# Performance work log

Hardware: AMD Instinct MI355X
Metric: run time of the kernel (lower is better)

Reference implementation:

```python
import jax, jax.numpy as jnp
import numpy as np

EPS_COMBINE = 1e-6   # F.normalize eps in embedder
EPS_FINAL = 1e-12    # F.normalize default eps


def _l2norm(x, eps):
    # torch F.normalize: x / max(||x||_2, eps)
    n = jnp.sqrt(jnp.sum(x * x, axis=-1, keepdims=True))
    return x / jnp.maximum(n, eps)


def setup_inputs() -> dict:
    key = jax.random.key(0)
    ks = jax.random.split(key, 6)
    B, H, E = 16384, 768, 8
    s1 = 1.0 / np.sqrt(H)
    s2 = 1.0 / np.sqrt(H // 2)
    return {
        "embedding": jax.random.normal(ks[0], (B, H), jnp.float32),
        "gate_logits": jax.random.normal(ks[1], (B, E), jnp.float32),
        "W1": jax.random.normal(ks[2], (E, H, H // 2), jnp.float32) * s1,
        "b1": jax.random.normal(ks[3], (E, H // 2), jnp.float32) * s1,
        "W2": jax.random.normal(ks[4], (E, H // 2, H), jnp.float32) * s2,
        "b2": jax.random.normal(ks[5], (E, H), jnp.float32) * s2,
    }


def reference(embedding, gate_logits, W1, b1, W2, b2):
    # cls(): softmax + top-1 mask (sbmoe_top1)
    p = jax.nn.softmax(gate_logits, axis=-1)               # [B, E]
    mask = jax.nn.one_hot(jnp.argmax(p, axis=-1), p.shape[-1], dtype=p.dtype)
    gate = p * mask                                        # [B, E]

    # embedder(): run EVERY expert (2-layer MLP) on all samples
    h = jax.nn.relu(jnp.einsum('bd,edh->beh', embedding, W1) + b1[None])  # [B, E, H/2]
    embs = jnp.einsum('beh,ehd->bed', h, W2) + b2[None]                   # [B, E, H]

    # weighted combine + normalize + residual
    combined = jnp.einsum('bed,be->bd', embs, gate)        # [B, H]
    out = _l2norm(combined, EPS_COMBINE) + embedding
    # normalize=True
    return _l2norm(out, EPS_FINAL)
```

## Files before the change

### kernel.cpp

```cpp
#include <hip/hip_runtime.h>
#include <hip/hip_bf16.h>
#include <stdint.h>

#define B_N   16384
#define H_DIM 768
#define HH    384
#define NE    8
#define CSTRIDE 32

typedef __attribute__((ext_vector_type(8))) short bf16x8;
typedef __attribute__((ext_vector_type(4))) float f32x4;

__device__ __forceinline__ unsigned short f2bf(float f) {
    uint32_t u = __float_as_uint(f);
    return (unsigned short)((u + 0x7fffu + ((u >> 16) & 1u)) >> 16);
}

__global__ void zero_counts_kernel(int* __restrict__ counts) {
    if (threadIdx.x < NE) counts[threadIdx.x * CSTRIDE] = 0;
}

__global__ void route_kernel(const float* __restrict__ logits,
                             int* __restrict__ counts,
                             int* __restrict__ buckets) {
    __shared__ int lcnt[NE];
    __shared__ int lbase[NE];
    const int tid = threadIdx.x;
    if (tid < NE) lcnt[tid] = 0;
    __syncthreads();

    const int b = blockIdx.x * 256 + tid;
    const float* l = logits + (size_t)b * NE;
    float best = l[0];
    int be = 0;
#pragma unroll
    for (int e = 1; e < NE; ++e) {
        float v = l[e];
        if (v > best) { best = v; be = e; }
    }
    const int lpos = atomicAdd(&lcnt[be], 1);
    __syncthreads();
    if (tid < NE) lbase[tid] = atomicAdd(&counts[tid * CSTRIDE], lcnt[tid]);
    __syncthreads();
    buckets[be * B_N + lbase[be] + lpos] = b;
}

__global__ void transpose_cvt_kernel(const float* __restrict__ W1,
                                     const float* __restrict__ W2,
                                     unsigned short* __restrict__ W1T,
                                     unsigned short* __restrict__ W2T,
                                     int* __restrict__ counts) {
    if (blockIdx.x == 0 && blockIdx.y == 0 && blockIdx.z == 0 && threadIdx.x < NE)
        counts[threadIdx.x * CSTRIDE] = 0;

    const int z = blockIdx.z;
    const int R = z ? HH : H_DIM;
    const int C = z ? H_DIM : HH;
    const float* src = (z ? W2 : W1) + (size_t)blockIdx.y * R * C;
    unsigned short* dst = (z ? W2T : W1T) + (size_t)blockIdx.y * R * C;

    const int ctiles = C >> 5;
    const int ty = blockIdx.x / ctiles;
    const int tx = blockIdx.x % ctiles;

    __shared__ float Ts[32][33];
    const int lr = threadIdx.x >> 3;
    const int lc = (threadIdx.x & 7) * 4;

    f32x4 v = *reinterpret_cast<const f32x4*>(src + (size_t)(ty * 32 + lr) * C + tx * 32 + lc);
    Ts[lr][lc + 0] = v[0]; Ts[lr][lc + 1] = v[1];
    Ts[lr][lc + 2] = v[2]; Ts[lr][lc + 3] = v[3];
    __syncthreads();

    ushort4 o;
    o.x = f2bf(Ts[lc + 0][lr]);
    o.y = f2bf(Ts[lc + 1][lr]);
    o.z = f2bf(Ts[lc + 2][lr]);
    o.w = f2bf(Ts[lc + 3][lr]);
    *reinterpret_cast<ushort4*>(dst + (size_t)(tx * 32 + lr) * R + ty * 32 + lc) = o;
}

template<int KTOT, int NTOT, bool A_F32, bool RELU_BF16>
__global__ __launch_bounds__(256, 4)
void gemm_kernel(const void* __restrict__ Aglob,
                 const unsigned short* __restrict__ WT,
                 const float* __restrict__ bias,
                 const int* __restrict__ counts,
                 const int* __restrict__ buckets,
                 void* __restrict__ Cout) {
    __shared__ __align__(16) unsigned char AsB[64 * 128];
    __shared__ __align__(16) unsigned char BsB[128 * 128];
    __shared__ int sidx[64];

    const int e      = blockIdx.y;
    const int cnt    = counts[e * CSTRIDE];
    const int mtile  = blockIdx.x & 255;
    const int nchunk = blockIdx.x >> 8;
    const int base   = mtile * 64;
    if (base >= cnt) return;
    const int ns  = min(64, cnt - base);
    const int tid = threadIdx.x;

    if (tid < 64) sidx[tid] = buckets[e * B_N + base + (tid < ns ? tid : 0)];
    __syncthreads();

    const int ar = tid >> 2, aq = tid & 3;
    const int bn = tid >> 1, bh = tid & 1;
    const float*          arow_f = nullptr;
    const unsigned short* arow_h = nullptr;
    if (A_F32) arow_f = (const float*)Aglob + (size_t)sidx[ar] * KTOT;
    else       arow_h = (const unsigned short*)Aglob + (size_t)sidx[ar] * KTOT;
    const unsigned short* brow =
        WT + ((size_t)e * NTOT + nchunk * 128 + bn) * KTOT;

    const int w = tid >> 6, lane = tid & 63;
    const int wr = w >> 1, wc = w & 1;
    const int fr = lane & 15, fq = lane >> 4;

    f32x4 acc[2][4];
#pragma unroll
    for (int mi = 0; mi < 2; ++mi)
#pragma unroll
        for (int ni = 0; ni < 4; ++ni) acc[mi][ni] = (f32x4)(0.f);

    for (int k0 = 0; k0 < KTOT; k0 += 64) {
        if (A_F32) {
            const float* ap = arow_f + k0 + aq * 16;
            f32x4 f0 = *reinterpret_cast<const f32x4*>(ap + 0);
            f32x4 f1 = *reinterpret_cast<const f32x4*>(ap + 4);
            f32x4 f2 = *reinterpret_cast<const f32x4*>(ap + 8);
            f32x4 f3 = *reinterpret_cast<const f32x4*>(ap + 12);
            bf16x8 p0, p1;
#pragma unroll
            for (int i = 0; i < 4; ++i) {
                p0[i]     = (short)f2bf(f0[i]);
                p0[i + 4] = (short)f2bf(f1[i]);
                p1[i]     = (short)f2bf(f2[i]);
                p1[i + 4] = (short)f2bf(f3[i]);
            }
            const int kb0 = aq * 32, sw = (ar & 7) << 4;
            *reinterpret_cast<bf16x8*>(&AsB[(ar << 7) + ((kb0)      ^ sw)]) = p0;
            *reinterpret_cast<bf16x8*>(&AsB[(ar << 7) + ((kb0 + 16) ^ sw)]) = p1;
        } else {
            const unsigned short* ap = arow_h + k0 + aq * 16;
            f32x4 c0 = *reinterpret_cast<const f32x4*>(ap + 0);
            f32x4 c1 = *reinterpret_cast<const f32x4*>(ap + 8);
            const int kb0 = aq * 32, sw = (ar & 7) << 4;
            *reinterpret_cast<f32x4*>(&AsB[(ar << 7) + ((kb0)      ^ sw)]) = c0;
            *reinterpret_cast<f32x4*>(&AsB[(ar << 7) + ((kb0 + 16) ^ sw)]) = c1;
        }
        {
            const unsigned short* bp = brow + k0 + bh * 32;
            f32x4 c0 = *reinterpret_cast<const f32x4*>(bp + 0);
            f32x4 c1 = *reinterpret_cast<const f32x4*>(bp + 8);
            f32x4 c2 = *reinterpret_cast<const f32x4*>(bp + 16);
            f32x4 c3 = *reinterpret_cast<const f32x4*>(bp + 24);
            const int kb0 = bh * 64, sw = (bn & 7) << 4;
            *reinterpret_cast<f32x4*>(&BsB[(bn << 7) + ((kb0)      ^ sw)]) = c0;
            *reinterpret_cast<f32x4*>(&BsB[(bn << 7) + ((kb0 + 16) ^ sw)]) = c1;
            *reinterpret_cast<f32x4*>(&BsB[(bn << 7) + ((kb0 + 32) ^ sw)]) = c2;
            *reinterpret_cast<f32x4*>(&BsB[(bn << 7) + ((kb0 + 48) ^ sw)]) = c3;
        }
        __syncthreads();

#pragma unroll
        for (int s = 0; s < 2; ++s) {
            bf16x8 af[2], bf[4];
            const int kb = s * 64 + fq * 16;
#pragma unroll
            for (int mi = 0; mi < 2; ++mi) {
                int row = wr * 32 + mi * 16 + fr;
                af[mi] = *reinterpret_cast<const bf16x8*>(&AsB[(row << 7) + (kb ^ ((row & 7) << 4))]);
            }
#pragma unroll
            for (int ni = 0; ni < 4; ++ni) {
                int row = wc * 64 + ni * 16 + fr;
                bf[ni] = *reinterpret_cast<const bf16x8*>(&BsB[(row << 7) + (kb ^ ((row & 7) << 4))]);
            }
#pragma unroll
            for (int mi = 0; mi < 2; ++mi)
#pragma unroll
                for (int ni = 0; ni < 4; ++ni)
                    acc[mi][ni] = __builtin_amdgcn_mfma_f32_16x16x32_bf16(
                        af[mi], bf[ni], acc[mi][ni], 0, 0, 0);
        }
        __syncthreads();
    }

    const float* be = bias + (size_t)e * NTOT + nchunk * 128 + wc * 64;
#pragma unroll
    for (int mi = 0; mi < 2; ++mi) {
        const int rl0 = wr * 32 + mi * 16 + fq * 4;
        int  sid[4];
        bool val[4];
#pragma unroll
        for (int r2 = 0; r2 < 4; ++r2) {
            int rl = rl0 + r2;
            val[r2] = (rl < ns);
            sid[r2] = sidx[rl];
        }
#pragma unroll
        for (int ni = 0; ni < 4; ++ni) {
            const int coll = ni * 16 + fr;
            const int colg = nchunk * 128 + wc * 64 + coll;
            const float bb = be[coll];
#pragma unroll
            for (int r2 = 0; r2 < 4; ++r2) {
                float v = acc[mi][ni][r2] + bb;
                if (RELU_BF16) {
                    v = fmaxf(v, 0.f);
                    if (val[r2])
                        ((unsigned short*)Cout)[(size_t)sid[r2] * NTOT + colg] = f2bf(v);
                } else {
                    if (val[r2])
                        ((float*)Cout)[(size_t)sid[r2] * NTOT + colg] = v;
                }
            }
        }
    }
}

__global__ void norm_kernel(const float* __restrict__ emb, float* __restrict__ out) {
    const int row  = blockIdx.x * 4 + (threadIdx.x >> 6);
    const int lane = threadIdx.x & 63;
    float* y = out + (size_t)row * H_DIM;
    const float* x = emb + (size_t)row * H_DIM;

    f32x4 yv[3], xv[3];
    float s1 = 0.f, s2 = 0.f, s3 = 0.f;
#pragma unroll
    for (int c = 0; c < 3; ++c) {
        int col = c * 256 + lane * 4;
        yv[c] = *reinterpret_cast<const f32x4*>(y + col);
        xv[c] = *reinterpret_cast<const f32x4*>(x + col);
#pragma unroll
        for (int i = 0; i < 4; ++i) {
            s1 = fmaf(yv[c][i], yv[c][i], s1);
            s2 = fmaf(yv[c][i], xv[c][i], s2);
            s3 = fmaf(xv[c][i], xv[c][i], s3);
        }
    }
#pragma unroll
    for (int m = 1; m < 64; m <<= 1) {
        s1 += __shfl_xor(s1, m);
        s2 += __shfl_xor(s2, m);
        s3 += __shfl_xor(s3, m);
    }
    const float n1 = fmaxf(sqrtf(s1), 1e-6f);
    const float i1 = 1.f / n1;
    const float t  = s1 * i1 * i1 + 2.f * s2 * i1 + s3;
    const float i2 = 1.f / fmaxf(sqrtf(t), 1e-12f);
#pragma unroll
    for (int c = 0; c < 3; ++c) {
        int col = c * 256 + lane * 4;
        f32x4 o;
#pragma unroll
        for (int i = 0; i < 4; ++i) o[i] = (yv[c][i] * i1 + xv[c][i]) * i2;
        *reinterpret_cast<f32x4*>(y + col) = o;
    }
}

#define TILE 64
#define NTHR 256
#define BK   64
__global__ __launch_bounds__(NTHR, 2)
void moe_fused_fallback(const float* __restrict__ emb,
                        const float* __restrict__ W1,
                        const float* __restrict__ b1,
                        const float* __restrict__ W2,
                        const float* __restrict__ b2,
                        const int* __restrict__ counts,
                        const int* __restrict__ buckets,
                        float* __restrict__ out) {
    __shared__ float Xs[TILE][BK];
    __shared__ __hip_bfloat16 Hs[TILE][HH];
    __shared__ int   sidx[TILE];
    __shared__ float s_in1[TILE];
    __shared__ float s_in2[TILE];

    const int e    = blockIdx.y;
    const int cnt  = counts[e * CSTRIDE];
    const int base = blockIdx.x * TILE;
    if (base >= cnt) return;
    const int ns = min(TILE, cnt - base);
    const int tid = threadIdx.x;
    const int sg  = tid >> 5;
    const int cg  = tid & 31;

    if (tid < TILE) sidx[tid] = buckets[e * B_N + base + ((tid < ns) ? tid : 0)];
    __syncthreads();

    float acc[8][12];
#pragma unroll
    for (int i = 0; i < 8; ++i)
#pragma unroll
        for (int j = 0; j < 12; ++j) acc[i][j] = 0.f;

    const float* W1e = W1 + (size_t)e * H_DIM * HH;
    const int r = tid >> 2, q = tid & 3;
    const float* xrow = emb + (size_t)sidx[r] * H_DIM;

    for (int kk = 0; kk < H_DIM; kk += BK) {
#pragma unroll
        for (int i = 0; i < 4; ++i)
            *reinterpret_cast<float4*>(&Xs[r][q * 16 + i * 4]) =
                *reinterpret_cast<const float4*>(xrow + kk + q * 16 + i * 4);
        __syncthreads();
#pragma unroll 2
        for (int k = 0; k < BK; ++k) {
            float xv[8], wv[12];
            const float* wrow = W1e + (size_t)(kk + k) * HH + cg;
#pragma unroll
            for (int j = 0; j < 12; ++j) wv[j] = wrow[j * 32];
#pragma unroll
            for (int i = 0; i < 8; ++i) xv[i] = Xs[sg * 8 + i][k];
#pragma unroll
            for (int i = 0; i < 8; ++i)
#pragma unroll
                for (int j = 0; j < 12; ++j) acc[i][j] = fmaf(xv[i], wv[j], acc[i][j]);
        }
        __syncthreads();
    }
    const float* b1e = b1 + e * HH;
#pragma unroll
    for (int j = 0; j < 12; ++j) {
        float bb = b1e[cg + j * 32];
#pragma unroll
        for (int i = 0; i < 8; ++i)
            Hs[sg * 8 + i][cg + j * 32] = __float2bfloat16(fmaxf(acc[i][j] + bb, 0.f));
    }
    __syncthreads();

    const float* W2e = W2 + (size_t)e * HH * H_DIM;
    const float* b2e = b2 + e * H_DIM;
    float S1[8], S2[8], S3[8];
#pragma unroll
    for (int i = 0; i < 8; ++i) { S1[i] = 0.f; S2[i] = 0.f; S3[i] = 0.f; }

    for (int hb = 0; hb < H_DIM; hb += 384) {
        float acc2[8][12];
#pragma unroll
        for (int i = 0; i < 8; ++i)
#pragma unroll
            for (int j = 0; j < 12; ++j) acc2[i][j] = 0.f;
#pragma unroll 2
        for (int k = 0; k < HH; ++k) {
            float hv[8], wv[12];
            const float* wrow = W2e + (size_t)k * H_DIM + hb + cg;
#pragma unroll
            for (int j = 0; j < 12; ++j) wv[j] = wrow[j * 32];
#pragma unroll
            for (int i = 0; i < 8; ++i) hv[i] = __bfloat162float(Hs[sg * 8 + i][k]);
#pragma unroll
            for (int i = 0; i < 8; ++i)
#pragma unroll
                for (int j = 0; j < 12; ++j) acc2[i][j] = fmaf(hv[i], wv[j], acc2[i][j]);
        }
#pragma unroll
        for (int j = 0; j < 12; ++j) {
            int col = hb + cg + j * 32;
            float bb = b2e[col];
#pragma unroll
            for (int i = 0; i < 8; ++i) {
                int s = sg * 8 + i;
                float y = acc2[i][j] + bb;
                size_t o = (size_t)sidx[s] * H_DIM + col;
                float x = emb[o];
                S1[i] = fmaf(y, y, S1[i]);
                S2[i] = fmaf(y, x, S2[i]);
                S3[i] = fmaf(x, x, S3[i]);
                if (s < ns) out[o] = y;
            }
        }
    }
#pragma unroll
    for (int i = 0; i < 8; ++i) {
        float v1 = S1[i], v2 = S2[i], v3 = S3[i];
#pragma unroll
        for (int m = 1; m < 32; m <<= 1) {
            v1 += __shfl_xor(v1, m); v2 += __shfl_xor(v2, m); v3 += __shfl_xor(v3, m);
        }
        if (cg == 0) {
            float n1 = fmaxf(sqrtf(v1), 1e-6f);
            float t  = v1 / (n1 * n1) + 2.f * v2 / n1 + v3;
            s_in1[sg * 8 + i] = 1.f / n1;
            s_in2[sg * 8 + i] = 1.f / fmaxf(sqrtf(t), 1e-12f);
        }
    }
    __syncthreads();
#pragma unroll
    for (int i = 0; i < 8; ++i) {
        int s = sg * 8 + i;
        if (s >= ns) continue;
        float in1 = s_in1[s], in2 = s_in2[s];
        size_t rowo = (size_t)sidx[s] * H_DIM;
#pragma unroll
        for (int j = 0; j < 24; ++j) {
            int col = cg + j * 32;
            out[rowo + col] = (out[rowo + col] * in1 + emb[rowo + col]) * in2;
        }
    }
}

extern "C" void kernel_launch(void* const* d_in, const int* in_sizes, int n_in,
                              void* d_out, int out_size, void* d_ws, size_t ws_size,
                              hipStream_t stream) {
    const float* emb    = (const float*)d_in[0];
    const float* logits = (const float*)d_in[1];
    const float* W1     = (const float*)d_in[2];
    const float* b1     = (const float*)d_in[3];
    const float* W2     = (const float*)d_in[4];
    const float* b2     = (const float*)d_in[5];
    float* out = (float*)d_out;

    int* counts  = (int*)d_ws;
    int* buckets = (int*)((char*)d_ws + 1024);
    unsigned short* W1T = (unsigned short*)((char*)d_ws + 1024 + 524288);
    unsigned short* W2T = W1T + (size_t)NE * HH * H_DIM;
    unsigned short* Hws = W2T + (size_t)NE * HH * H_DIM;
    const size_t needed = 1024 + 524288
                        + 2 * (size_t)NE * HH * H_DIM * sizeof(unsigned short)
                        + (size_t)B_N * HH * sizeof(unsigned short);

    if (ws_size >= needed) {
        transpose_cvt_kernel<<<dim3(288, NE, 2), 256, 0, stream>>>(W1, W2, W1T, W2T, counts);
        route_kernel<<<B_N / 256, 256, 0, stream>>>(logits, counts, buckets);
        gemm_kernel<H_DIM, HH, true, true>
            <<<dim3(256 * 3, NE), 256, 0, stream>>>(emb, W1T, b1, counts, buckets, Hws);
        gemm_kernel<HH, H_DIM, false, false>
            <<<dim3(256 * 6, NE), 256, 0, stream>>>(Hws, W2T, b2, counts, buckets, out);
        norm_kernel<<<B_N / 4, 256, 0, stream>>>(emb, out);
    } else {
        zero_counts_kernel<<<1, 64, 0, stream>>>(counts);
        route_kernel<<<B_N / 256, 256, 0, stream>>>(logits, counts, buckets);
        moe_fused_fallback<<<dim3(B_N / TILE, NE), NTHR, 0, stream>>>(
            emb, W1, b1, W2, b2, counts, buckets, out);
    }
}
```

Baseline: 214.8 us.

## Double-buffer GEMM LDS with 512-thread blocks, interleaved expert grid, bf16 second-layer output

The expert GEMM moves to 512 threads with register-staged global loads and double-buffered LDS, so the next K tile loads while the current one feeds the MFMAs. The grid is flattened with the expert index in the low bits so blocks from different experts interleave. When the workspace is large enough, the second GEMM writes bf16 into the workspace and the norm kernel reads bf16, halving that intermediate traffic. The cost is some precision on the pre-normalisation output and more LDS per block, which may lower occupancy.

```diff
diff --git a/kernel.cpp b/kernel.cpp
--- a/kernel.cpp
+++ b/kernel.cpp
@@ -80,22 +80,24 @@
     *reinterpret_cast<ushort4*>(dst + (size_t)(tx * 32 + lr) * R + ty * 32 + lc) = o;
 }
 
-template<int KTOT, int NTOT, bool A_F32, bool RELU_BF16>
-__global__ __launch_bounds__(256, 4)
+template<int KTOT, int NTOT, bool A_F32, bool RELU, bool OUTBF>
+__global__ __launch_bounds__(512, 6)
 void gemm_kernel(const void* __restrict__ Aglob,
                  const unsigned short* __restrict__ WT,
                  const float* __restrict__ bias,
                  const int* __restrict__ counts,
                  const int* __restrict__ buckets,
                  void* __restrict__ Cout) {
-    __shared__ __align__(16) unsigned char AsB[64 * 128];
-    __shared__ __align__(16) unsigned char BsB[128 * 128];
+    __shared__ __align__(16) unsigned char AsB[2][64 * 128];
+    __shared__ __align__(16) unsigned char BsB[2][128 * 128];
     __shared__ int sidx[64];
 
-    const int e      = blockIdx.y;
+    const int wgid   = blockIdx.x;
+    const int e      = wgid & 7;
+    const int rest   = wgid >> 3;
+    const int mtile  = rest & 255;
+    const int nchunk = rest >> 8;
     const int cnt    = counts[e * CSTRIDE];
-    const int mtile  = blockIdx.x & 255;
-    const int nchunk = blockIdx.x >> 8;
     const int base   = mtile * 64;
     if (base >= cnt) return;
     const int ns  = min(64, cnt - base);
@@ -104,159 +106,187 @@
     if (tid < 64) sidx[tid] = buckets[e * B_N + base + (tid < ns ? tid : 0)];
     __syncthreads();
 
-    const int ar = tid >> 2, aq = tid & 3;
-    const int bn = tid >> 1, bh = tid & 1;
+    const int ar = tid >> 3, aq = tid & 7;
+    const int bn = tid >> 2, bq = tid & 3;
     const float*          arow_f = nullptr;
     const unsigned short* arow_h = nullptr;
-    if (A_F32) arow_f = (const float*)Aglob + (size_t)sidx[ar] * KTOT;
-    else       arow_h = (const unsigned short*)Aglob + (size_t)sidx[ar] * KTOT;
+    if (A_F32) arow_f = (const float*)Aglob + (size_t)sidx[ar] * KTOT + aq * 8;
+    else       arow_h = (const unsigned short*)Aglob + (size_t)sidx[ar] * KTOT + aq * 8;
     const unsigned short* brow =
-        WT + ((size_t)e * NTOT + nchunk * 128 + bn) * KTOT;
+        WT + ((size_t)e * NTOT + nchunk * 128 + bn) * KTOT + bq * 16;
+
+    const int a_slot  = (ar << 7) + ((aq * 16) ^ ((ar & 7) << 4));
+    const int b_slot0 = (bn << 7) + (((bq * 32)     ) ^ ((bn & 7) << 4));
+    const int b_slot1 = (bn << 7) + (((bq * 32) + 16) ^ ((bn & 7) << 4));
 
     const int w = tid >> 6, lane = tid & 63;
-    const int wr = w >> 1, wc = w & 1;
+    const int wr = w >> 2, wc = w & 3;
     const int fr = lane & 15, fq = lane >> 4;
 
-    f32x4 acc[2][4];
+    f32x4 acc[2][2];
 #pragma unroll
     for (int mi = 0; mi < 2; ++mi)
 #pragma unroll
-        for (int ni = 0; ni < 4; ++ni) acc[mi][ni] = (f32x4)(0.f);
-
-    for (int k0 = 0; k0 < KTOT; k0 += 64) {
+        for (int ni = 0; ni < 2; ++ni) acc[mi][ni] = (f32x4)(0.f);
+
+    bf16x8 aReg;
+    f32x4  bReg0, bReg1;
+
+    auto LOAD = [&](int k0) {
         if (A_F32) {
-            const float* ap = arow_f + k0 + aq * 16;
-            f32x4 f0 = *reinterpret_cast<const f32x4*>(ap + 0);
-            f32x4 f1 = *reinterpret_cast<const f32x4*>(ap + 4);
-            f32x4 f2 = *reinterpret_cast<const f32x4*>(ap + 8);
-            f32x4 f3 = *reinterpret_cast<const f32x4*>(ap + 12);
-            bf16x8 p0, p1;
+            f32x4 f0 = *reinterpret_cast<const f32x4*>(arow_f + k0);
+            f32x4 f1 = *reinterpret_cast<const f32x4*>(arow_f + k0 + 4);
+            bf16x8 p;
 #pragma unroll
             for (int i = 0; i < 4; ++i) {
-                p0[i]     = (short)f2bf(f0[i]);
-                p0[i + 4] = (short)f2bf(f1[i]);
-                p1[i]     = (short)f2bf(f2[i]);
-                p1[i + 4] = (short)f2bf(f3[i]);
-            }
-            const int kb0 = aq * 32, sw = (ar & 7) << 4;
-            *reinterpret_cast<bf16x8*>(&AsB[(ar << 7) + ((kb0)      ^ sw)]) = p0;
-            *reinterpret_cast<bf16x8*>(&AsB[(ar << 7) + ((kb0 + 16) ^ sw)]) = p1;
+                p[i]     = (short)f2bf(f0[i]);
+                p[i + 4] = (short)f2bf(f1[i]);
+            }
+            aReg = p;
         } else {
-            const unsigned short* ap = arow_h + k0 + aq * 16;
-            f32x4 c0 = *reinterpret_cast<const f32x4*>(ap + 0);
-            f32x4 c1 = *reinterpret_cast<const f32x4*>(ap + 8);
-            const int kb0 = aq * 32, sw = (ar & 7) << 4;
-            *reinterpret_cast<f32x4*>(&AsB[(ar << 7) + ((kb0)      ^ sw)]) = c0;
-            *reinterpret_cast<f32x4*>(&AsB[(ar << 7) + ((kb0 + 16) ^ sw)]) = c1;
-        }
-        {
-            const unsigned short* bp = brow + k0 + bh * 32;
-            f32x4 c0 = *reinterpret_cast<const f32x4*>(bp + 0);
-            f32x4 c1 = *reinterpret_cast<const f32x4*>(bp + 8);
-            f32x4 c2 = *reinterpret_cast<const f32x4*>(bp + 16);
-            f32x4 c3 = *reinterpret_cast<const f32x4*>(bp + 24);
-            const int kb0 = bh * 64, sw = (bn & 7) << 4;
-            *reinterpret_cast<f32x4*>(&BsB[(bn << 7) + ((kb0)      ^ sw)]) = c0;
-            *reinterpret_cast<f32x4*>(&BsB[(bn << 7) + ((kb0 + 16) ^ sw)]) = c1;
-            *reinterpret_cast<f32x4*>(&BsB[(bn << 7) + ((kb0 + 32) ^ sw)]) = c2;
-            *reinterpret_cast<f32x4*>(&BsB[(bn << 7) + ((kb0 + 48) ^ sw)]) = c3;
-        }
-        __syncthreads();
-
+            aReg = *reinterpret_cast<const bf16x8*>(arow_h + k0);
+        }
+        bReg0 = *reinterpret_cast<const f32x4*>(brow + k0);
+        bReg1 = *reinterpret_cast<const f32x4*>(brow + k0 + 8);
+    };
+    auto WRITE = [&](int buf) {
+        *reinterpret_cast<bf16x8*>(&AsB[buf][a_slot])  = aReg;
+        *reinterpret_cast<f32x4*>(&BsB[buf][b_slot0]) = bReg0;
+        *reinterpret_cast<f32x4*>(&BsB[buf][b_slot1]) = bReg1;
+    };
+    auto COMPUTE = [&](int buf) {
 #pragma unroll
         for (int s = 0; s < 2; ++s) {
-            bf16x8 af[2], bf[4];
             const int kb = s * 64 + fq * 16;
+            bf16x8 af[2], bfr[2];
 #pragma unroll
             for (int mi = 0; mi < 2; ++mi) {
                 int row = wr * 32 + mi * 16 + fr;
-                af[mi] = *reinterpret_cast<const bf16x8*>(&AsB[(row << 7) + (kb ^ ((row & 7) << 4))]);
-            }
-#pragma unroll
-            for (int ni = 0; ni < 4; ++ni) {
-                int row = wc * 64 + ni * 16 + fr;
-                bf[ni] = *reinterpret_cast<const bf16x8*>(&BsB[(row << 7) + (kb ^ ((row & 7) << 4))]);
+                af[mi] = *reinterpret_cast<const bf16x8*>(
+                    &AsB[buf][(row << 7) + (kb ^ ((row & 7) << 4))]);
+            }
+#pragma unroll
+            for (int ni = 0; ni < 2; ++ni) {
+                int row = wc * 32 + ni * 16 + fr;
+                bfr[ni] = *reinterpret_cast<const bf16x8*>(
+                    &BsB[buf][(row << 7) + (kb ^ ((row & 7) << 4))]);
             }
 #pragma unroll
             for (int mi = 0; mi < 2; ++mi)
 #pragma unroll
-                for (int ni = 0; ni < 4; ++ni)
+                for (int ni = 0; ni < 2; ++ni)
                     acc[mi][ni] = __builtin_amdgcn_mfma_f32_16x16x32_bf16(
-                        af[mi], bf[ni], acc[mi][ni], 0, 0, 0);
-        }
+                        af[mi], bfr[ni], acc[mi][ni], 0, 0, 0);
+        }
+    };
+
+    LOAD(0);
+    WRITE(0);
+    __syncthreads();
+    int cur = 0;
+    for (int k0 = 64; k0 < KTOT; k0 += 64) {
+        LOAD(k0);
+        COMPUTE(cur);
+        WRITE(cur ^ 1);
         __syncthreads();
-    }
-
-    const float* be = bias + (size_t)e * NTOT + nchunk * 128 + wc * 64;
+        cur ^= 1;
+    }
+    COMPUTE(cur);
+
+    const float* be = bias + (size_t)e * NTOT + nchunk * 128 + wc * 32;
 #pragma unroll
     for (int mi = 0; mi < 2; ++mi) {
         const int rl0 = wr * 32 + mi * 16 + fq * 4;
-        int  sid[4];
-        bool val[4];
-#pragma unroll
-        for (int r2 = 0; r2 < 4; ++r2) {
-            int rl = rl0 + r2;
-            val[r2] = (rl < ns);
-            sid[r2] = sidx[rl];
-        }
-#pragma unroll
-        for (int ni = 0; ni < 4; ++ni) {
+#pragma unroll
+        for (int ni = 0; ni < 2; ++ni) {
             const int coll = ni * 16 + fr;
-            const int colg = nchunk * 128 + wc * 64 + coll;
+            const int colg = nchunk * 128 + wc * 32 + coll;
             const float bb = be[coll];
 #pragma unroll
             for (int r2 = 0; r2 < 4; ++r2) {
-                float v = acc[mi][ni][r2] + bb;
-                if (RELU_BF16) {
-                    v = fmaxf(v, 0.f);
-                    if (val[r2])
-                        ((unsigned short*)Cout)[(size_t)sid[r2] * NTOT + colg] = f2bf(v);
-                } else {
-                    if (val[r2])
-                        ((float*)Cout)[(size_t)sid[r2] * NTOT + colg] = v;
+                const int rl = rl0 + r2;
+                if (rl < ns) {
+                    float v = acc[mi][ni][r2] + bb;
+                    if (RELU) v = fmaxf(v, 0.f);
+                    size_t o = (size_t)sidx[rl] * NTOT + colg;
+                    if (OUTBF) ((unsigned short*)Cout)[o] = f2bf(v);
+                    else       ((float*)Cout)[o] = v;
                 }
             }
         }
     }
 }
 
-__global__ void norm_kernel(const float* __restrict__ emb, float* __restrict__ out) {
+template<bool YB>
+__global__ void norm_kernel(const float* __restrict__ emb,
+                            const unsigned short* __restrict__ y2b,
+                            float* __restrict__ out) {
     const int row  = blockIdx.x * 4 + (threadIdx.x >> 6);
     const int lane = threadIdx.x & 63;
-    float* y = out + (size_t)row * H_DIM;
     const float* x = emb + (size_t)row * H_DIM;
-
-    f32x4 yv[3], xv[3];
+    float* o = out + (size_t)row * H_DIM;
+
     float s1 = 0.f, s2 = 0.f, s3 = 0.f;
-#pragma unroll
-    for (int c = 0; c < 3; ++c) {
-        int col = c * 256 + lane * 4;
-        yv[c] = *reinterpret_cast<const f32x4*>(y + col);
-        xv[c] = *reinterpret_cast<const f32x4*>(x + col);
-#pragma unroll
-        for (int i = 0; i < 4; ++i) {
-            s1 = fmaf(yv[c][i], yv[c][i], s1);
-            s2 = fmaf(yv[c][i], xv[c][i], s2);
-            s3 = fmaf(xv[c][i], xv[c][i], s3);
-        }
-    }
-#pragma unroll
-    for (int m = 1; m < 64; m <<= 1) {
-        s1 += __shfl_xor(s1, m);
-        s2 += __shfl_xor(s2, m);
-        s3 += __shfl_xor(s3, m);
-    }
-    const float n1 = fmaxf(sqrtf(s1), 1e-6f);
-    const float i1 = 1.f / n1;
-    const float t  = s1 * i1 * i1 + 2.f * s2 * i1 + s3;
-    const float i2 = 1.f / fmaxf(sqrtf(t), 1e-12f);
-#pragma unroll
-    for (int c = 0; c < 3; ++c) {
-        int col = c * 256 + lane * 4;
-        f32x4 o;
-#pragma unroll
-        for (int i = 0; i < 4; ++i) o[i] = (yv[c][i] * i1 + xv[c][i]) * i2;
-        *reinterpret_cast<f32x4*>(y + col) = o;
+    if (YB) {
+        const uint32_t* yrow = reinterpret_cast<const uint32_t*>(y2b + (size_t)row * H_DIM);
+        float y0v[6], y1v[6];
+        float2 xv[6];
+#pragma unroll
+        for (int c = 0; c < 6; ++c) {
+            uint32_t u = yrow[c * 64 + lane];
+            float y0 = __uint_as_float(u << 16);
+            float y1 = __uint_as_float(u & 0xffff0000u);
+            float2 xx = *reinterpret_cast<const float2*>(x + 2 * (c * 64 + lane));
+            y0v[c] = y0; y1v[c] = y1; xv[c] = xx;
+            s1 = fmaf(y0, y0, s1); s1 = fmaf(y1, y1, s1);
+            s2 = fmaf(y0, xx.x, s2); s2 = fmaf(y1, xx.y, s2);
+            s3 = fmaf(xx.x, xx.x, s3); s3 = fmaf(xx.y, xx.y, s3);
+        }
+#pragma unroll
+        for (int m = 1; m < 64; m <<= 1) {
+            s1 += __shfl_xor(s1, m); s2 += __shfl_xor(s2, m); s3 += __shfl_xor(s3, m);
+        }
+        const float n1 = fmaxf(sqrtf(s1), 1e-6f);
+        const float i1 = 1.f / n1;
+        const float t  = s1 * i1 * i1 + 2.f * s2 * i1 + s3;
+        const float i2 = 1.f / fmaxf(sqrtf(t), 1e-12f);
+#pragma unroll
+        for (int c = 0; c < 6; ++c) {
+            float2 ov;
+            ov.x = (y0v[c] * i1 + xv[c].x) * i2;
+            ov.y = (y1v[c] * i1 + xv[c].y) * i2;
+            *reinterpret_cast<float2*>(o + 2 * (c * 64 + lane)) = ov;
+        }
+    } else {
+        f32x4 yv[3], xv[3];
+#pragma unroll
+        for (int c = 0; c < 3; ++c) {
+            int col = c * 256 + lane * 4;
+            yv[c] = *reinterpret_cast<const f32x4*>(o + col);
+            xv[c] = *reinterpret_cast<const f32x4*>(x + col);
+#pragma unroll
+            for (int i = 0; i < 4; ++i) {
+                s1 = fmaf(yv[c][i], yv[c][i], s1);
+                s2 = fmaf(yv[c][i], xv[c][i], s2);
+                s3 = fmaf(xv[c][i], xv[c][i], s3);
+            }
+        }
+#pragma unroll
+        for (int m = 1; m < 64; m <<= 1) {
+            s1 += __shfl_xor(s1, m); s2 += __shfl_xor(s2, m); s3 += __shfl_xor(s3, m);
+        }
+        const float n1 = fmaxf(sqrtf(s1), 1e-6f);
+        const float i1 = 1.f / n1;
+        const float t  = s1 * i1 * i1 + 2.f * s2 * i1 + s3;
+        const float i2 = 1.f / fmaxf(sqrtf(t), 1e-12f);
+#pragma unroll
+        for (int c = 0; c < 3; ++c) {
+            int col = c * 256 + lane * 4;
+            f32x4 ov;
+#pragma unroll
+            for (int i = 0; i < 4; ++i) ov[i] = (yv[c][i] * i1 + xv[c][i]) * i2;
+            *reinterpret_cast<f32x4*>(o + col) = ov;
+        }
     }
 }
 
@@ -415,21 +445,29 @@
 
     int* counts  = (int*)d_ws;
     int* buckets = (int*)((char*)d_ws + 1024);
-    unsigned short* W1T = (unsigned short*)((char*)d_ws + 1024 + 524288);
-    unsigned short* W2T = W1T + (size_t)NE * HH * H_DIM;
-    unsigned short* Hws = W2T + (size_t)NE * HH * H_DIM;
-    const size_t needed = 1024 + 524288
-                        + 2 * (size_t)NE * HH * H_DIM * sizeof(unsigned short)
-                        + (size_t)B_N * HH * sizeof(unsigned short);
-
-    if (ws_size >= needed) {
+    unsigned short* W1T  = (unsigned short*)((char*)d_ws + 1024 + 524288);
+    unsigned short* W2T  = W1T + (size_t)NE * HH * H_DIM;
+    unsigned short* Hws  = W2T + (size_t)NE * HH * H_DIM;
+    unsigned short* y2ws = Hws + (size_t)B_N * HH;
+    const size_t need_base = 1024 + 524288
+                           + 2 * (size_t)NE * HH * H_DIM * sizeof(unsigned short)
+                           + (size_t)B_N * HH * sizeof(unsigned short);
+    const size_t need_bf16 = need_base + (size_t)B_N * H_DIM * sizeof(unsigned short);
+
+    if (ws_size >= need_base) {
         transpose_cvt_kernel<<<dim3(288, NE, 2), 256, 0, stream>>>(W1, W2, W1T, W2T, counts);
         route_kernel<<<B_N / 256, 256, 0, stream>>>(logits, counts, buckets);
-        gemm_kernel<H_DIM, HH, true, true>
-            <<<dim3(256 * 3, NE), 256, 0, stream>>>(emb, W1T, b1, counts, buckets, Hws);
-        gemm_kernel<HH, H_DIM, false, false>
-            <<<dim3(256 * 6, NE), 256, 0, stream>>>(Hws, W2T, b2, counts, buckets, out);
-        norm_kernel<<<B_N / 4, 256, 0, stream>>>(emb, out);
+        gemm_kernel<H_DIM, HH, true, true, true>
+            <<<NE * 256 * 3, 512, 0, stream>>>(emb, W1T, b1, counts, buckets, Hws);
+        if (ws_size >= need_bf16) {
+            gemm_kernel<HH, H_DIM, false, false, true>
+                <<<NE * 256 * 6, 512, 0, stream>>>(Hws, W2T, b2, counts, buckets, y2ws);
+            norm_kernel<true><<<B_N / 4, 256, 0, stream>>>(emb, y2ws, out);
+        } else {
+            gemm_kernel<HH, H_DIM, false, false, false>
+                <<<NE * 256 * 6, 512, 0, stream>>>(Hws, W2T, b2, counts, buckets, out);
+            norm_kernel<false><<<B_N / 4, 256, 0, stream>>>(emb, nullptr, out);
+        }
     } else {
         zero_counts_kernel<<<1, 64, 0, stream>>>(counts);
         route_kernel<<<B_N / 256, 256, 0, stream>>>(logits, counts, buckets);
```

Measured after the change: 186.2 us. 13.3% less time.
